# Performance work log

Hardware: AMD Instinct MI355X
Metric: run time of the kernel (lower is better)

## Reference

```python
import jax, jax.numpy as jnp
import numpy as np

NUM_HEADS = 16
NUM_KV_GROUPS = 4
EPS = 1e-6


def _rms_norm(x, w):
    # normalize over last dim (head_dim)
    return x * jax.lax.rsqrt(jnp.mean(x * x, axis=-1, keepdims=True) + EPS) * w


def _rope_cos_sin(T, head_dim):
    half = head_dim // 2
    inv_freq = 1.0 / (10000.0 ** (jnp.arange(half, dtype=jnp.float32) / half))
    freqs = jnp.arange(T, dtype=jnp.float32)[:, None] * inv_freq[None, :]  # [T, half]
    cos = jnp.repeat(jnp.cos(freqs), 2, axis=-1)  # [T, head_dim]
    sin = jnp.repeat(jnp.sin(freqs), 2, axis=-1)
    return cos, sin


def _apply_rope(x, cos, sin):
    # x: [B, H, T, head_dim]; cos/sin broadcast over B,H
    x1 = x[..., ::2]
    x2 = x[..., 1::2]
    x_rot = jnp.stack([-x2, x1], axis=-1).reshape(x.shape)  # interleave (-x2, x1)
    return x * cos + x_rot * sin


def setup_inputs() -> dict:
    key = jax.random.key(0)
    ks = jax.random.split(key, 5)
    scale = lambda k, sh: jax.random.normal(k, sh, dtype=jnp.float32) * 0.02
    return {
        "x": jax.random.normal(ks[0], (4, 2048, 1024), dtype=jnp.float32),
        "Wq": scale(ks[1], (1024, 1024)),
        "Wk": scale(ks[2], (256, 1024)),
        "Wv": scale(ks[3], (256, 1024)),
        "Wo": scale(ks[4], (1024, 1024)),
        "qn_w": jnp.ones((64,), jnp.float32),
        "kn_w": jnp.ones((64,), jnp.float32),
    }


def reference(x, Wq, Wk, Wv, Wo, qn_w, kn_w):
    B, T, D = x.shape
    H, G = NUM_HEADS, NUM_KV_GROUPS
    hd = D // H

    # projections (torch Linear: y = x @ W.T), reshape to [B, heads, T, hd]
    q = (x @ Wq.T).reshape(B, T, H, hd).transpose(0, 2, 1, 3)
    k = (x @ Wk.T).reshape(B, T, G, hd).transpose(0, 2, 1, 3)
    v = (x @ Wv.T).reshape(B, T, G, hd).transpose(0, 2, 1, 3)

    # optional qk RMSNorm (qk_norm=True)
    q = _rms_norm(q, qn_w)
    k = _rms_norm(k, kn_w)

    # RoPE (position_offset = 0)
    cos, sin = _rope_cos_sin(T, hd)
    q = _apply_rope(q, cos, sin)
    k = _apply_rope(k, cos, sin)

    # GQA: expand kv heads to match query heads
    rep = H // G
    k = jnp.repeat(k, rep, axis=1)
    v = jnp.repeat(v, rep, axis=1)

    # causal SDPA
    scores = jnp.einsum('bhqd,bhkd->bhqk', q, k) / jnp.sqrt(jnp.float32(hd))
    causal = jnp.tril(jnp.ones((T, T), dtype=bool))
    scores = jnp.where(causal, scores, jnp.float32(-1e30))
    attn = jax.nn.softmax(scores, axis=-1)
    out = jnp.einsum('bhqk,bhkd->bhqd', attn, v)

    out = out.transpose(0, 2, 1, 3).reshape(B, T, D)
    return out @ Wo.T
```

## Files before the change

### kernel.cpp

```cpp
#include <hip/hip_runtime.h>

typedef unsigned short u16;
typedef __attribute__((ext_vector_type(8))) short bf16x8;
typedef __attribute__((ext_vector_type(4))) short bf16x4;
typedef __attribute__((ext_vector_type(4))) float f32x4;

#define GP(p) ((const __attribute__((address_space(1))) void*)(unsigned long long)(p))
#define LP(p) ((__attribute__((address_space(3))) void*)(unsigned int)(unsigned long long)(p))

#define QSCALE 0.180336879486998f
#define M_BIAS (-12.0f)

__device__ __forceinline__ u16 f2bf(float f) {
  union { float f; unsigned u; } v; v.f = f;
  unsigned r = v.u + 0x7fffu + ((v.u >> 16) & 1u);
  return (u16)(r >> 16);
}
__device__ __forceinline__ short f2bf_cvt(float f) {
  __bf16 b = (__bf16)f;
  return *reinterpret_cast<short*>(&b);
}

#if __has_builtin(__builtin_amdgcn_mfma_f32_16x16x16bf16_1k)
#define MFMA16(A, B, C) __builtin_amdgcn_mfma_f32_16x16x16bf16_1k((A), (B), (C), 0, 0, 0)
#elif __has_builtin(__builtin_amdgcn_mfma_f32_16x16x16_bf16)
#define MFMA16(A, B, C) __builtin_amdgcn_mfma_f32_16x16x16_bf16((A), (B), (C), 0, 0, 0)
#else
static __device__ __forceinline__ f32x4 mfma16_asm(bf16x4 a, bf16x4 b, f32x4 c) {
  asm volatile("v_mfma_f32_16x16x16_bf16 %0, %1, %2, %0" : "+v"(c) : "v"(a), "v"(b));
  return c;
}
#define MFMA16(A, B, C) mfma16_asm((A), (B), (C))
#endif

__global__ void cast_kernel(const float* __restrict__ in, u16* __restrict__ out, int n4) {
  int i = blockIdx.x * blockDim.x + threadIdx.x;
  int stride = gridDim.x * blockDim.x;
  for (; i < n4; i += stride) {
    float4 v = reinterpret_cast<const float4*>(in)[i];
    ushort4 o = make_ushort4(f2bf(v.x), f2bf(v.y), f2bf(v.z), f2bf(v.w));
    reinterpret_cast<ushort4*>(out)[i] = o;
  }
}

__global__ void cast_w_kernel(const float* __restrict__ Wq, const float* __restrict__ Wk,
                              const float* __restrict__ Wv, const float* __restrict__ Wo,
                              u16* __restrict__ Wcat, u16* __restrict__ Wob) {
  int i = blockIdx.x * 256 + threadIdx.x;
  const float* src; u16* dst; int off;
  if (i < 262144)      { src = Wq; dst = Wcat;           off = i; }
  else if (i < 327680) { src = Wk; dst = Wcat + 1048576; off = i - 262144; }
  else if (i < 393216) { src = Wv; dst = Wcat + 1310720; off = i - 327680; }
  else                 { src = Wo; dst = Wob;            off = i - 393216; }
  float4 v = reinterpret_cast<const float4*>(src)[off];
  reinterpret_cast<ushort4*>(dst)[off] =
      make_ushort4(f2bf(v.x), f2bf(v.y), f2bf(v.z), f2bf(v.w));
}

__global__ void rope_table_kernel(float* __restrict__ ctab, float* __restrict__ stab) {
  int i = blockIdx.x * 256 + threadIdx.x;
  int t = i >> 5, f = i & 31;
  float inv = exp2f((float)f * (-13.287712379549449f / 32.0f));
  float ang = (float)t * inv;
  float sv, cv;
  sincosf(ang, &sv, &cv);
  ctab[i] = cv;
  stab[i] = sv;
}

__launch_bounds__(256)
__global__ void gemm_qkv_kernel(const u16* __restrict__ A, const u16* __restrict__ W,
                                u16* __restrict__ qh, u16* __restrict__ kh,
                                u16* __restrict__ vt,
                                const float* __restrict__ qn_w, const float* __restrict__ kn_w,
                                const float* __restrict__ ctab, const float* __restrict__ stab) {
  __shared__ __align__(16) u16 As[128 * 64];
  __shared__ __align__(16) u16 Bs[128 * 64];
  const int tid = threadIdx.x;
  const int w = tid >> 6, l = tid & 63;
  const int lr = l & 15, lk = l >> 4;
  const int wr = w >> 1, wc = w & 1;
  const int m0 = blockIdx.x * 128, n0 = blockIdx.y * 128;
  f32x4 acc[4][4] = {};
  for (int k0 = 0; k0 < 1024; k0 += 64) {
#pragma unroll
    for (int i = 0; i < 4; ++i) {
      int c = i * 256 + tid;
      const u16* ga = A + (size_t)(m0 + (c >> 3)) * 1024 + k0 + (c & 7) * 8;
      __builtin_amdgcn_global_load_lds(GP(ga), LP((char*)As + (i * 256 + (tid & ~63)) * 16), 16, 0, 0);
      const u16* gb = W + (size_t)(n0 + (c >> 3)) * 1024 + k0 + (c & 7) * 8;
      __builtin_amdgcn_global_load_lds(GP(gb), LP((char*)Bs + (i * 256 + (tid & ~63)) * 16), 16, 0, 0);
    }
    asm volatile("s_waitcnt vmcnt(0)" ::: "memory");
    __syncthreads();
#pragma unroll
    for (int kk = 0; kk < 2; ++kk) {
      bf16x8 af[4], bfr[4];
#pragma unroll
      for (int fi = 0; fi < 4; ++fi)
        af[fi] = *reinterpret_cast<const bf16x8*>(&As[(wr * 64 + fi * 16 + lr) * 64 + kk * 32 + lk * 8]);
#pragma unroll
      for (int fj = 0; fj < 4; ++fj)
        bfr[fj] = *reinterpret_cast<const bf16x8*>(&Bs[(wc * 64 + fj * 16 + lr) * 64 + kk * 32 + lk * 8]);
#pragma unroll
      for (int fi = 0; fi < 4; ++fi)
#pragma unroll
        for (int fj = 0; fj < 4; ++fj)
          acc[fi][fj] = __builtin_amdgcn_mfma_f32_16x16x32_bf16(af[fi], bfr[fj], acc[fi][fj], 0, 0, 0);
    }
    __syncthreads();
  }
  const int ncol0 = n0 + wc * 64;
  if (ncol0 < 1280) {
    const bool isq = ncol0 < 1024;
    const float* wn = isq ? qn_w : kn_w;
    const float sc = isq ? QSCALE : 1.0f;
    float wv[4];
#pragma unroll
    for (int fj = 0; fj < 4; ++fj) wv[fj] = wn[fj * 16 + lr];
#pragma unroll
    for (int fi = 0; fi < 4; ++fi)
#pragma unroll
      for (int r = 0; r < 4; ++r) {
        float ss = 0.f;
#pragma unroll
        for (int fj = 0; fj < 4; ++fj) ss += acc[fi][fj][r] * acc[fi][fj][r];
        ss += __shfl_xor(ss, 1); ss += __shfl_xor(ss, 2);
        ss += __shfl_xor(ss, 4); ss += __shfl_xor(ss, 8);
        float rinv = rsqrtf(ss * (1.0f / 64.0f) + 1e-6f);
        int m = m0 + wr * 64 + fi * 16 + lk * 4 + r;
        int t = m & 2047, b = m >> 11;
#pragma unroll
        for (int fj = 0; fj < 4; ++fj) {
          float xn = acc[fi][fj][r] * rinv * wv[fj];
          float pr = __shfl_xor(xn, 1);
          float rot = (lr & 1) ? pr : -pr;
          int ci = t * 32 + fj * 8 + (lr >> 1);
          u16 outv = f2bf((xn * ctab[ci] + rot * stab[ci]) * sc);
          int n = ncol0 + fj * 16 + lr;
          if (isq) {
            int h = n >> 6, d = n & 63;
            qh[((size_t)((b * 16 + h) * 2048 + t)) * 64 + d] = outv;
          } else {
            int n2 = n - 1024, g = n2 >> 6, d = n2 & 63;
            kh[((size_t)((b * 4 + g) * 2048 + t)) * 64 + d] = outv;
          }
        }
      }
  } else {
#pragma unroll
    for (int fi = 0; fi < 4; ++fi)
#pragma unroll
      for (int fj = 0; fj < 4; ++fj) {
        int m = m0 + wr * 64 + fi * 16 + lk * 4;
        int b = m >> 11, t = m & 2047;
        int n2 = ncol0 + fj * 16 + lr - 1280;
        int g = n2 >> 6, d = n2 & 63;
        bf16x4 o;
#pragma unroll
        for (int r = 0; r < 4; ++r) o[r] = f2bf_cvt(acc[fi][fj][r]);
        *reinterpret_cast<bf16x4*>(&vt[((size_t)((b * 4 + g) * 64 + d)) * 2048 + t]) = o;
      }
  }
}

__launch_bounds__(512)
__global__ void attn_kernel(const u16* __restrict__ qh, const u16* __restrict__ kh,
                            const u16* __restrict__ vt, u16* __restrict__ ao) {
  __shared__ __align__(16) u16 Ks[2][64 * 64];
  __shared__ __align__(16) u16 Vts[2][64 * 64];
  const int tid = threadIdx.x, w = tid >> 6, l = tid & 63;
  const int lr = l & 15, lk = l >> 4;
  const int wq = w & 3, wh = w >> 2;
  const int D = blockIdx.x;
  const int j = D >> 3;
  const int p = j & 15, hp = (j >> 4) & 1;
  const int z = (D & 7) + 8 * (j >> 5);
  const int b = z >> 2, g = z & 3;
  const int h = g * 4 + hp * 2 + wh;
  const u16* Qh = qh + ((size_t)((b * 16 + h) * 2048)) * 64;
  const u16* Kb = kh + ((size_t)z * 2048) * 64;
  const u16* Vtb = vt + ((size_t)z * 64) * 2048;
  const int swz = (lr & 7) * 8;

  const int r0 = tid >> 3, s0 = ((tid & 7) ^ (r0 & 7)) * 8;
  char* kd = (char*)&Ks[0][0] + (tid & ~63) * 16;
  char* vd = (char*)&Vts[0][0] + (tid & ~63) * 16;
  const u16* kp; const u16* vp;

  auto stage = [&](int buf) {
    __builtin_amdgcn_global_load_lds(GP(kp), LP(kd + buf * 8192), 16, 0, 0);
    __builtin_amdgcn_global_load_lds(GP(vp), LP(vd + buf * 8192), 16, 0, 0);
    kp += 64 * 64; vp += 64;
  };

  int cur = 0;
  auto run_qtile = [&](int qt) {
    const int q0 = qt * 64;
    const u16* Qb = Qh + (size_t)(q0 + wq * 16) * 64;
    const bf16x8 qf0 = *reinterpret_cast<const bf16x8*>(&Qb[lr * 64 + lk * 8]);
    const bf16x8 qf1 = *reinterpret_cast<const bf16x8*>(&Qb[lr * 64 + 32 + lk * 8]);
    f32x4 oacc[4] = {};
    float lrow = 0.f;
    kp = Kb + r0 * 64 + s0;
    vp = Vtb + (size_t)r0 * 2048 + s0;
    stage(cur);
    asm volatile("s_waitcnt vmcnt(0)" ::: "memory");
    __builtin_amdgcn_s_barrier();
    for (int it = 0; it <= qt; ++it) {
      if (it < qt) stage(cur ^ 1);
      f32x4 sacc[4];
#pragma unroll
      for (int fi = 0; fi < 4; ++fi)
#pragma unroll
        for (int r = 0; r < 4; ++r) sacc[fi][r] = M_BIAS;
      __builtin_amdgcn_s_setprio(1);
#pragma unroll
      for (int kk = 0; kk < 2; ++kk) {
        bf16x8 qf = kk ? qf1 : qf0;
#pragma unroll
        for (int fi = 0; fi < 4; ++fi) {
          bf16x8 kf = *reinterpret_cast<const bf16x8*>(
              &Ks[cur][(fi * 16 + lr) * 64 + ((kk * 32 + lk * 8) ^ swz)]);
          sacc[fi] = __builtin_amdgcn_mfma_f32_16x16x32_bf16(kf, qf, sacc[fi], 0, 0, 0);
        }
      }
      __builtin_amdgcn_s_setprio(0);
      if (it == qt) {
        int qloc = wq * 16 + lr;
#pragma unroll
        for (int fi = 0; fi < 4; ++fi)
#pragma unroll
          for (int r = 0; r < 4; ++r)
            if (fi * 16 + lk * 4 + r > qloc) sacc[fi][r] = -1e30f;
      }
      bf16x4 pb[4];
#pragma unroll
      for (int fi = 0; fi < 4; ++fi)
#pragma unroll
        for (int r = 0; r < 4; ++r) {
          float pv = exp2f(sacc[fi][r]);
          lrow += pv;
          pb[fi][r] = f2bf_cvt(pv);
        }
      __builtin_amdgcn_s_setprio(1);
#pragma unroll
      for (int fi = 0; fi < 4; ++fi)
#pragma unroll
        for (int db = 0; db < 4; ++db) {
          bf16x4 vf = *reinterpret_cast<const bf16x4*>(
              &Vts[cur][(db * 16 + lr) * 64 + ((fi * 16 + lk * 4) ^ swz)]);
          oacc[db] = MFMA16(vf, pb[fi], oacc[db]);
        }
      __builtin_amdgcn_s_setprio(0);
      asm volatile("s_waitcnt vmcnt(0)" ::: "memory");
      __builtin_amdgcn_s_barrier();
      cur ^= 1;
    }
    float lsum = lrow;
    lsum += __shfl_xor(lsum, 16);
    lsum += __shfl_xor(lsum, 32);
    float inv = 1.0f / lsum;
#pragma unroll
    for (int db = 0; db < 4; ++db) {
      bf16x4 o;
#pragma unroll
      for (int r = 0; r < 4; ++r) o[r] = f2bf_cvt(oacc[db][r] * inv);
      *reinterpret_cast<bf16x4*>(
          &ao[((size_t)(b * 2048 + q0 + wq * 16 + lr)) * 1024 + h * 64 + db * 16 + lk * 4]) = o;
    }
  };
  run_qtile(31 - p);
  run_qtile(p);
}

__launch_bounds__(256)
__global__ void gemm_out_kernel(const u16* __restrict__ A, const u16* __restrict__ W,
                                float* __restrict__ out) {
  __shared__ __align__(16) u16 As[128 * 64];
  __shared__ __align__(16) u16 Bs[128 * 64];
  const int tid = threadIdx.x;
  const int w = tid >> 6, l = tid & 63;
  const int lr = l & 15, lk = l >> 4;
  const int wr = w >> 1, wc = w & 1;
  const int m0 = blockIdx.x * 128, n0 = blockIdx.y * 128;
  f32x4 acc[4][4] = {};
  for (int k0 = 0; k0 < 1024; k0 += 64) {
#pragma unroll
    for (int i = 0; i < 4; ++i) {
      int c = i * 256 + tid;
      const u16* ga = A + (size_t)(m0 + (c >> 3)) * 1024 + k0 + (c & 7) * 8;
      __builtin_amdgcn_global_load_lds(GP(ga), LP((char*)As + (i * 256 + (tid & ~63)) * 16), 16, 0, 0);
      const u16* gb = W + (size_t)(n0 + (c >> 3)) * 1024 + k0 + (c & 7) * 8;
      __builtin_amdgcn_global_load_lds(GP(gb), LP((char*)Bs + (i * 256 + (tid & ~63)) * 16), 16, 0, 0);
    }
    asm volatile("s_waitcnt vmcnt(0)" ::: "memory");
    __syncthreads();
#pragma unroll
    for (int kk = 0; kk < 2; ++kk) {
      bf16x8 af[4], bfr[4];
#pragma unroll
      for (int fi = 0; fi < 4; ++fi)
        af[fi] = *reinterpret_cast<const bf16x8*>(&As[(wr * 64 + fi * 16 + lr) * 64 + kk * 32 + lk * 8]);
#pragma unroll
      for (int fj = 0; fj < 4; ++fj)
        bfr[fj] = *reinterpret_cast<const bf16x8*>(&Bs[(wc * 64 + fj * 16 + lr) * 64 + kk * 32 + lk * 8]);
#pragma unroll
      for (int fi = 0; fi < 4; ++fi)
#pragma unroll
        for (int fj = 0; fj < 4; ++fj)
          acc[fi][fj] = __builtin_amdgcn_mfma_f32_16x16x32_bf16(af[fi], bfr[fj], acc[fi][fj], 0, 0, 0);
    }
    __syncthreads();
  }
#pragma unroll
  for (int fi = 0; fi < 4; ++fi)
#pragma unroll
    for (int fj = 0; fj < 4; ++fj)
#pragma unroll
      for (int r = 0; r < 4; ++r) {
        int m = m0 + wr * 64 + fi * 16 + lk * 4 + r;
        int n = n0 + wc * 64 + fj * 16 + lr;
        out[(size_t)m * 1024 + n] = acc[fi][fj][r];
      }
}

extern "C" void kernel_launch(void* const* d_in, const int* in_sizes, int n_in,
                              void* d_out, int out_size, void* d_ws, size_t ws_size,
                              hipStream_t stream) {
  const float* x  = (const float*)d_in[0];
  const float* Wq = (const float*)d_in[1];
  const float* Wk = (const float*)d_in[2];
  const float* Wv = (const float*)d_in[3];
  const float* Wo = (const float*)d_in[4];
  const float* qn = (const float*)d_in[5];
  const float* kn = (const float*)d_in[6];
  float* out = (float*)d_out;
  char* ws = (char*)d_ws;
  u16* xb   = (u16*)(ws);
  u16* Wcat = (u16*)(ws + 16777216);
  u16* Wob  = (u16*)(ws + 19922944);
  u16* qh   = (u16*)(ws + 22020096);
  u16* kh   = (u16*)(ws + 38797312);
  u16* vtb  = (u16*)(ws + 42991616);
  u16* ao   = (u16*)(ws + 47185920);
  float* ctab = (float*)ao;
  float* stab = ctab + 65536;

  cast_kernel<<<2048, 256, 0, stream>>>(x, xb, 8388608 / 4);
  cast_w_kernel<<<2560, 256, 0, stream>>>(Wq, Wk, Wv, Wo, Wcat, Wob);
  rope_table_kernel<<<256, 256, 0, stream>>>(ctab, stab);
  dim3 g1(64, 12);
  gemm_qkv_kernel<<<g1, 256, 0, stream>>>(xb, Wcat, qh, kh, vtb, qn, kn, ctab, stab);
  attn_kernel<<<512, 512, 0, stream>>>(qh, kh, vtb, ao);
  dim3 g2(64, 8);
  gemm_out_kernel<<<g2, 256, 0, stream>>>(ao, Wob, out);
}
```

Before: 171.5 us.

## Merge prep kernels into one launch and double-buffer output GEMM loads

The three preprocessing kernels (x cast, weight cast, RoPE table) are merged into a single launch that dispatches on block index, removing two kernel launches and their inter-kernel gaps. The output projection GEMM now double-buffers its LDS tiles, issuing the next K-slice's global-to-LDS loads before computing on the current one, and raises wave priority around the MFMA section. This is meant to hide global load latency behind MFMA work. It doubles the LDS footprint of the output GEMM, which may reduce occupancy.

```diff
diff --git a/kernel.cpp b/kernel.cpp
--- a/kernel.cpp
+++ b/kernel.cpp
@@ -33,39 +33,40 @@
 #define MFMA16(A, B, C) mfma16_asm((A), (B), (C))
 #endif
 
-__global__ void cast_kernel(const float* __restrict__ in, u16* __restrict__ out, int n4) {
-  int i = blockIdx.x * blockDim.x + threadIdx.x;
-  int stride = gridDim.x * blockDim.x;
-  for (; i < n4; i += stride) {
-    float4 v = reinterpret_cast<const float4*>(in)[i];
-    ushort4 o = make_ushort4(f2bf(v.x), f2bf(v.y), f2bf(v.z), f2bf(v.w));
-    reinterpret_cast<ushort4*>(out)[i] = o;
-  }
-}
-
-__global__ void cast_w_kernel(const float* __restrict__ Wq, const float* __restrict__ Wk,
-                              const float* __restrict__ Wv, const float* __restrict__ Wo,
-                              u16* __restrict__ Wcat, u16* __restrict__ Wob) {
-  int i = blockIdx.x * 256 + threadIdx.x;
-  const float* src; u16* dst; int off;
-  if (i < 262144)      { src = Wq; dst = Wcat;           off = i; }
-  else if (i < 327680) { src = Wk; dst = Wcat + 1048576; off = i - 262144; }
-  else if (i < 393216) { src = Wv; dst = Wcat + 1310720; off = i - 327680; }
-  else                 { src = Wo; dst = Wob;            off = i - 393216; }
-  float4 v = reinterpret_cast<const float4*>(src)[off];
-  reinterpret_cast<ushort4*>(dst)[off] =
-      make_ushort4(f2bf(v.x), f2bf(v.y), f2bf(v.z), f2bf(v.w));
-}
-
-__global__ void rope_table_kernel(float* __restrict__ ctab, float* __restrict__ stab) {
-  int i = blockIdx.x * 256 + threadIdx.x;
-  int t = i >> 5, f = i & 31;
-  float inv = exp2f((float)f * (-13.287712379549449f / 32.0f));
-  float ang = (float)t * inv;
-  float sv, cv;
-  sincosf(ang, &sv, &cv);
-  ctab[i] = cv;
-  stab[i] = sv;
+__global__ void prep_kernel(const float* __restrict__ x,
+                            const float* __restrict__ Wq, const float* __restrict__ Wk,
+                            const float* __restrict__ Wv, const float* __restrict__ Wo,
+                            u16* __restrict__ xb, u16* __restrict__ Wcat,
+                            u16* __restrict__ Wob,
+                            float* __restrict__ ctab, float* __restrict__ stab) {
+  const int bid = blockIdx.x, tid = threadIdx.x;
+  if (bid < 2048) {
+    for (int i = bid * 256 + tid; i < 2097152; i += 2048 * 256) {
+      float4 v = reinterpret_cast<const float4*>(x)[i];
+      reinterpret_cast<ushort4*>(xb)[i] =
+          make_ushort4(f2bf(v.x), f2bf(v.y), f2bf(v.z), f2bf(v.w));
+    }
+  } else if (bid < 2688) {
+    for (int i = (bid - 2048) * 256 + tid; i < 655360; i += 640 * 256) {
+      const float* src; u16* dst; int off;
+      if (i < 262144)      { src = Wq; dst = Wcat;           off = i; }
+      else if (i < 327680) { src = Wk; dst = Wcat + 1048576; off = i - 262144; }
+      else if (i < 393216) { src = Wv; dst = Wcat + 1310720; off = i - 327680; }
+      else                 { src = Wo; dst = Wob;            off = i - 393216; }
+      float4 v = reinterpret_cast<const float4*>(src)[off];
+      reinterpret_cast<ushort4*>(dst)[off] =
+          make_ushort4(f2bf(v.x), f2bf(v.y), f2bf(v.z), f2bf(v.w));
+    }
+  } else {
+    int i = (bid - 2688) * 256 + tid;
+    int t = i >> 5, f = i & 31;
+    float inv = exp2f((float)f * (-13.287712379549449f / 32.0f));
+    float ang = (float)t * inv;
+    float sv, cv;
+    sincosf(ang, &sv, &cv);
+    ctab[i] = cv;
+    stab[i] = sv;
+  }
 }
 
 __launch_bounds__(256)
@@ -277,41 +278,60 @@
 __launch_bounds__(256)
 __global__ void gemm_out_kernel(const u16* __restrict__ A, const u16* __restrict__ W,
                                 float* __restrict__ out) {
-  __shared__ __align__(16) u16 As[128 * 64];
-  __shared__ __align__(16) u16 Bs[128 * 64];
+  __shared__ __align__(16) u16 As[2][128 * 64];
+  __shared__ __align__(16) u16 Bs[2][128 * 64];
   const int tid = threadIdx.x;
   const int w = tid >> 6, l = tid & 63;
   const int lr = l & 15, lk = l >> 4;
   const int wr = w >> 1, wc = w & 1;
   const int m0 = blockIdx.x * 128, n0 = blockIdx.y * 128;
+  const u16* ap[4];
+  const u16* bp[4];
+#pragma unroll
+  for (int i = 0; i < 4; ++i) {
+    int c = i * 256 + tid;
+    ap[i] = A + (size_t)(m0 + (c >> 3)) * 1024 + (c & 7) * 8;
+    bp[i] = W + (size_t)(n0 + (c >> 3)) * 1024 + (c & 7) * 8;
+  }
+  auto stage = [&](int buf) {
+#pragma unroll
+    for (int i = 0; i < 4; ++i) {
+      __builtin_amdgcn_global_load_lds(GP(ap[i]),
+          LP((char*)&As[0][0] + buf * 16384 + (i * 256 + (tid & ~63)) * 16), 16, 0, 0);
+      __builtin_amdgcn_global_load_lds(GP(bp[i]),
+          LP((char*)&Bs[0][0] + buf * 16384 + (i * 256 + (tid & ~63)) * 16), 16, 0, 0);
+      ap[i] += 64; bp[i] += 64;
+    }
+  };
   f32x4 acc[4][4] = {};
+  int cur = 0;
+  stage(0);
+  asm volatile("s_waitcnt vmcnt(0)" ::: "memory");
+  __builtin_amdgcn_s_barrier();
   for (int k0 = 0; k0 < 1024; k0 += 64) {
-#pragma unroll
-    for (int i = 0; i < 4; ++i) {
-      int c = i * 256 + tid;
-      const u16* ga = A + (size_t)(m0 + (c >> 3)) * 1024 + k0 + (c & 7) * 8;
-      __builtin_amdgcn_global_load_lds(GP(ga), LP((char*)As + (i * 256 + (tid & ~63)) * 16), 16, 0, 0);
-      const u16* gb = W + (size_t)(n0 + (c >> 3)) * 1024 + k0 + (c & 7) * 8;
-      __builtin_amdgcn_global_load_lds(GP(gb), LP((char*)Bs + (i * 256 + (tid & ~63)) * 16), 16, 0, 0);
-    }
-    asm volatile("s_waitcnt vmcnt(0)" ::: "memory");
-    __syncthreads();
+    if (k0 < 960) stage(cur ^ 1);
+    __builtin_amdgcn_s_setprio(1);
 #pragma unroll
     for (int kk = 0; kk < 2; ++kk) {
       bf16x8 af[4], bfr[4];
 #pragma unroll
       for (int fi = 0; fi < 4; ++fi)
-        af[fi] = *reinterpret_cast<const bf16x8*>(&As[(wr * 64 + fi * 16 + lr) * 64 + kk * 32 + lk * 8]);
+        af[fi] = *reinterpret_cast<const bf16x8*>(
+            &As[cur][(wr * 64 + fi * 16 + lr) * 64 + kk * 32 + lk * 8]);
 #pragma unroll
       for (int fj = 0; fj < 4; ++fj)
-        bfr[fj] = *reinterpret_cast<const bf16x8*>(&Bs[(wc * 64 + fj * 16 + lr) * 64 + kk * 32 + lk * 8]);
+        bfr[fj] = *reinterpret_cast<const bf16x8*>(
+            &Bs[cur][(wc * 64 + fj * 16 + lr) * 64 + kk * 32 + lk * 8]);
 #pragma unroll
       for (int fi = 0; fi < 4; ++fi)
 #pragma unroll
         for (int fj = 0; fj < 4; ++fj)
           acc[fi][fj] = __builtin_amdgcn_mfma_f32_16x16x32_bf16(af[fi], bfr[fj], acc[fi][fj], 0, 0, 0);
     }
-    __syncthreads();
+    __builtin_amdgcn_s_setprio(0);
+    asm volatile("s_waitcnt vmcnt(0)" ::: "memory");
+    __builtin_amdgcn_s_barrier();
+    cur ^= 1;
   }
 #pragma unroll
   for (int fi = 0; fi < 4; ++fi)
@@ -347,9 +367,7 @@
   float* ctab = (float*)ao;
   float* stab = ctab + 65536;
 
-  cast_kernel<<<2048, 256, 0, stream>>>(x, xb, 8388608 / 4);
-  cast_w_kernel<<<2560, 256, 0, stream>>>(Wq, Wk, Wv, Wo, Wcat, Wob);
-  rope_table_kernel<<<256, 256, 0, stream>>>(ctab, stab);
+  prep_kernel<<<2944, 256, 0, stream>>>(x, Wq, Wk, Wv, Wo, xb, Wcat, Wob, ctab, stab);
   dim3 g1(64, 12);
   gemm_qkv_kernel<<<g1, 256, 0, stream>>>(xb, Wcat, qh, kh, vtb, qn, kn, ctab, stab);
   attn_kernel<<<512, 512, 0, stream>>>(qh, kh, vtb, ao);
```

Measured after the change: 165.3 us. 3.6% less time.
